# Optimization experiments

Hardware: AMD Instinct MI355X
Metric: run time of the kernel (lower is better)

## Reference

```python
import jax, jax.numpy as jnp
import numpy as np
from jax import lax

B = 8; IMG = 224; P = 16; D = 192; DEPTH = 8
H = IMG // P; W = H; L = H * W
D_IN = 384; D_STATE = 16; D_CONV = 4; DT_R = 12; NCLS = 1000
EPS = 1e-5


def _ln(x, w, b):
    m = x.mean(-1, keepdims=True)
    v = ((x - m) ** 2).mean(-1, keepdims=True)
    return (x - m) * lax.rsqrt(v + EPS) * w + b


def _mixer(seq, p):
    # seq: (B, L, D) -> Mamba selective-scan mixer
    xz = jnp.einsum('bld,ed->ble', seq, p['in_proj_w'])  # (B,L,2*D_IN)
    u, z = jnp.split(xz, 2, axis=-1)
    # causal depthwise conv1d over L
    uc = lax.conv_general_dilated(u.transpose(0, 2, 1), p['conv_w'][:, None, :], (1,),
                                  [(D_CONV - 1, 0)], feature_group_count=D_IN,
                                  dimension_numbers=('NCH', 'OIH', 'NCH'))
    u = jax.nn.silu(uc.transpose(0, 2, 1) + p['conv_b'])
    xdbl = jnp.einsum('bld,ed->ble', u, p['x_proj_w'])  # (B,L,DT_R+2*D_STATE)
    dt = xdbl[..., :DT_R]
    Bm = xdbl[..., DT_R:DT_R + D_STATE]
    Cm = xdbl[..., DT_R + D_STATE:]
    delta = jax.nn.softplus(jnp.einsum('blr,dr->bld', dt, p['dt_w']) + p['dt_b'])
    A = -jnp.exp(p['A_log'])  # (D_IN, D_STATE)

    def step(h, inp):
        d_t, B_t, C_t, u_t = inp  # (b,D_IN),(b,N),(b,N),(b,D_IN)
        h = h * jnp.exp(d_t[..., None] * A) + (d_t * u_t)[..., None] * B_t[:, None, :]
        return h, jnp.einsum('bdn,bn->bd', h, C_t)

    h0 = jnp.zeros((seq.shape[0], D_IN, D_STATE), seq.dtype)
    _, ys = lax.scan(step, h0, (delta.transpose(1, 0, 2), Bm.transpose(1, 0, 2),
                                Cm.transpose(1, 0, 2), u.transpose(1, 0, 2)))
    y = ys.transpose(1, 0, 2) + u * p['D']
    y = y * jax.nn.silu(z)
    return jnp.einsum('bld,cd->blc', y, p['out_proj_w'])


def _stack(seq, params):
    # Block: residual = residual + hidden; hidden = mixer(LN(residual))
    def body(carry, p):
        hidden, residual = carry
        residual = residual + hidden
        hidden = _mixer(_ln(residual, p['ln_w'], p['ln_b']), p)
        return (hidden, residual), None

    (hidden, residual), _ = lax.scan(body, (seq, jnp.zeros_like(seq)), params)
    return hidden + residual


def _forward(x, patch_w, patch_b, pe_ln_w, pe_ln_b, ln_w, ln_b, in_proj_w, conv_w,
             conv_b, x_proj_w, dt_w, dt_b, A_log, Dp, out_proj_w, out_norm_w,
             out_norm_b, head_ln_w, head_ln_b, head_w, head_b):
    b = x.shape[0]
    # patch embed: conv(stride=patch) + LayerNorm over channels
    feat = lax.conv_general_dilated(x, patch_w, (P, P), 'VALID',
                                    dimension_numbers=('NCHW', 'OIHW', 'NCHW'))
    feat = feat + patch_b[None, :, None, None]  # (B, D, H, W)
    feat = _ln(feat.transpose(0, 2, 3, 1), pe_ln_w, pe_ln_b).transpose(0, 3, 1, 2)
    # CrossScan: 4 directional unrollings
    x0 = feat.reshape(b, D, L)
    x1 = feat.transpose(0, 1, 3, 2).reshape(b, D, L)
    xs = jnp.stack([x0, x1, x0[..., ::-1], x1[..., ::-1]], axis=1)  # (B,4,D,L)
    dirs = xs.transpose(1, 0, 3, 2)  # (4,B,L,D)
    params = {'ln_w': ln_w, 'ln_b': ln_b, 'in_proj_w': in_proj_w, 'conv_w': conv_w,
              'conv_b': conv_b, 'x_proj_w': x_proj_w, 'dt_w': dt_w, 'dt_b': dt_b,
              'A_log': A_log, 'D': Dp, 'out_proj_w': out_proj_w}
    outs = jax.vmap(_stack)(dirs, params)  # (4,B,L,D)
    # CrossMerge
    ys = outs.transpose(1, 0, 3, 2)  # (B,4,D,L)
    ym = ys[:, 0:2] + ys[:, 2:4][..., ::-1]
    y = ym[:, 0] + ym[:, 1].reshape(b, D, W, H).transpose(0, 1, 3, 2).reshape(b, D, L)
    y = _ln(y.transpose(0, 2, 1), out_norm_w, out_norm_b)  # (B,L,D)
    y = _ln(y.reshape(b, H, W, D), head_ln_w, head_ln_b)
    return y.mean(axis=(1, 2)) @ head_w.T + head_b  # (B, NCLS)


def setup_inputs() -> dict:
    key = jax.random.key(0)
    ks = jax.random.split(key, 10)
    rn = lambda k, s, sc=0.02: jax.random.normal(k, s, jnp.float32) * sc
    A_init = jnp.broadcast_to(jnp.arange(1, D_STATE + 1, dtype=jnp.float32),
                              (4, DEPTH, D_IN, D_STATE))
    return {
        'x': jax.random.normal(ks[0], (B, 3, IMG, IMG), jnp.float32),
        'patch_w': rn(ks[1], (D, 3, P, P)),
        'patch_b': jnp.zeros((D,), jnp.float32),
        'pe_ln_w': jnp.ones((D,), jnp.float32),
        'pe_ln_b': jnp.zeros((D,), jnp.float32),
        'ln_w': jnp.ones((4, DEPTH, D), jnp.float32),
        'ln_b': jnp.zeros((4, DEPTH, D), jnp.float32),
        'in_proj_w': rn(ks[2], (4, DEPTH, 2 * D_IN, D)),
        'conv_w': rn(ks[3], (4, DEPTH, D_IN, D_CONV), 0.1),
        'conv_b': jnp.zeros((4, DEPTH, D_IN), jnp.float32),
        'x_proj_w': rn(ks[4], (4, DEPTH, DT_R + 2 * D_STATE, D_IN)),
        'dt_w': rn(ks[5], (4, DEPTH, D_IN, DT_R), 0.1),
        'dt_b': jnp.log(jnp.expm1(0.01)) + rn(ks[6], (4, DEPTH, D_IN), 0.02),
        'A_log': jnp.log(A_init),
        'Dp': jnp.ones((4, DEPTH, D_IN), jnp.float32),
        'out_proj_w': rn(ks[7], (4, DEPTH, D, D_IN)),
        'out_norm_w': jnp.ones((D,), jnp.float32),
        'out_norm_b': jnp.zeros((D,), jnp.float32),
        'head_ln_w': jnp.ones((D,), jnp.float32),
        'head_ln_b': jnp.zeros((D,), jnp.float32),
        'head_w': rn(ks[8], (NCLS, D)),
        'head_b': jnp.zeros((NCLS,), jnp.float32),
    }


def reference(x, patch_w, patch_b, pe_ln_w, pe_ln_b, ln_w, ln_b, in_proj_w, conv_w,
              conv_b, x_proj_w, dt_w, dt_b, A_log, Dp, out_proj_w, out_norm_w,
              out_norm_b, head_ln_w, head_ln_b, head_w, head_b):
    return _forward(x, patch_w, patch_b, pe_ln_w, pe_ln_b, ln_w, ln_b, in_proj_w,
                    conv_w, conv_b, x_proj_w, dt_w, dt_b, A_log, Dp, out_proj_w,
                    out_norm_w, out_norm_b, head_ln_w, head_ln_b, head_w, head_b)
```

## Files before the change

kernel.cpp:

```cpp
#include <hip/hip_runtime.h>

#define B_ 8
#define IMGSZ 224
#define PATCH 16
#define D_ 192
#define DEPTH_ 8
#define H_ 14
#define W_ 14
#define L_ 196
#define DIN 384
#define DSTATE 16
#define DCONV 4
#define DTR 12
#define NCLS_ 1000
#define EPS_ 1e-5f
#define ROWS_PER_DIR (B_*L_)
#define M_TOTAL (4*ROWS_PER_DIR)

typedef unsigned short ushort_t;
typedef unsigned int uint_t;
typedef __attribute__((ext_vector_type(8)))  short bf16x8;
typedef __attribute__((ext_vector_type(16))) float f32x16;

__device__ __forceinline__ ushort_t f2bf(float f) {
  uint_t u = __builtin_bit_cast(uint_t, f);
  u += 0x7fffu + ((u >> 16) & 1u);
  return (ushort_t)(u >> 16);
}
__device__ __forceinline__ float bf2f(ushort_t s) {
  uint_t u = ((uint_t)s) << 16;
  return __builtin_bit_cast(float, u);
}

__global__ __launch_bounds__(256) void k_cvt3(
    const float* __restrict__ s0, const float* __restrict__ s1,
    const float* __restrict__ s2, ushort_t* __restrict__ dst)
{
  int i = blockIdx.x*256 + threadIdx.x;
  if (i >= 1806336) return;
  const float* src;
  int off;
  if (i < 36864)        { src = s0; off = i; }
  else if (i < 1216512) { src = s1; off = i - 36864; }
  else                  { src = s2; off = i - 1216512; }
  float4 v = reinterpret_cast<const float4*>(src)[off];
  ushort4 o;
  o.x = f2bf(v.x); o.y = f2bf(v.y); o.z = f2bf(v.z); o.w = f2bf(v.w);
  reinterpret_cast<ushort4*>(dst)[i] = o;
}

__global__ __launch_bounds__(256) void k_cvt_xw(const float* __restrict__ src,
                                                ushort_t* __restrict__ dst)
{
  int idx = blockIdx.x*256 + threadIdx.x;
  if (idx >= 32*64*384) return;
  int g = idx / (64*384);
  int r = (idx / 384) % 64;
  int k = idx % 384;
  float v = (r < 44) ? src[((size_t)g*44 + r)*384 + k] : 0.f;
  dst[idx] = f2bf(v);
}

__global__ __launch_bounds__(256) void k_im2col(const float* __restrict__ x,
                                                ushort_t* __restrict__ Xp)
{
  int idx = blockIdx.x*256 + threadIdx.x;
  if (idx >= ROWS_PER_DIR*768) return;
  int row = idx / 768, k = idx - row*768;
  int b = row / L_, l = row - b*L_;
  int hh = l / W_, ww = l - hh*W_;
  int c = k >> 8, rem = k & 255, pi = rem >> 4, pj = rem & 15;
  float v = x[(((size_t)b*3 + c)*IMGSZ + hh*PATCH + pi)*IMGSZ + ww*PATCH + pj];
  Xp[idx] = f2bf(v);
}

template<int KT, int OBF>
__global__ __launch_bounds__(64) void k_gemm2(
    const ushort_t* __restrict__ X, const ushort_t* __restrict__ W,
    void* __restrict__ C, int N, int nb, int wstride, int rows_per_dir)
{
  int row0 = blockIdx.x*32, col0 = blockIdx.y*64;
  int dir = row0 / rows_per_dir;
  const ushort_t* Wp = W + (size_t)dir*wstride;
  int l = threadIdx.x;
  int r31 = l & 31, khalf = (l >> 5)*8;
  const ushort_t* aptr  = X  + (size_t)(row0 + r31)*KT + khalf;
  const ushort_t* b0ptr = Wp + (size_t)(col0 + r31)*KT + khalf;
  const ushort_t* b1ptr = b0ptr + (size_t)32*KT;
  f32x16 acc00 = {}, acc01 = {}, acc10 = {}, acc11 = {};
  #pragma unroll
  for (int k = 0; k < KT; k += 32) {
    bf16x8 a0 = *reinterpret_cast<const bf16x8*>(aptr + k);
    bf16x8 a1 = *reinterpret_cast<const bf16x8*>(aptr + k + 16);
    bf16x8 b00 = *reinterpret_cast<const bf16x8*>(b0ptr + k);
    bf16x8 b01 = *reinterpret_cast<const bf16x8*>(b0ptr + k + 16);
    bf16x8 b10 = *reinterpret_cast<const bf16x8*>(b1ptr + k);
    bf16x8 b11 = *reinterpret_cast<const bf16x8*>(b1ptr + k + 16);
    acc00 = __builtin_amdgcn_mfma_f32_32x32x16_bf16(a0, b00, acc00, 0, 0, 0);
    acc01 = __builtin_amdgcn_mfma_f32_32x32x16_bf16(a1, b01, acc01, 0, 0, 0);
    acc10 = __builtin_amdgcn_mfma_f32_32x32x16_bf16(a0, b10, acc10, 0, 0, 0);
    acc11 = __builtin_amdgcn_mfma_f32_32x32x16_bf16(a1, b11, acc11, 0, 0, 0);
  }
  int c0 = col0 + r31, c1 = col0 + 32 + r31;
  #pragma unroll
  for (int r = 0; r < 16; ++r) {
    int row = (r & 3) + 8*(r >> 2) + 4*(l >> 5);
    size_t base = (size_t)(row0 + row)*N;
    float v0 = acc00[r] + acc01[r];
    float v1 = acc10[r] + acc11[r];
    if (OBF) {
      ushort_t* crow = (ushort_t*)C + base;
      if (c0 < nb) crow[c0] = f2bf(v0);
      if (c1 < nb) crow[c1] = f2bf(v1);
    } else {
      float* crow = (float*)C + base;
      if (c0 < nb) crow[c0] = v0;
      if (c1 < nb) crow[c1] = v1;
    }
  }
}

__global__ __launch_bounds__(64) void k_peln(
    const float* __restrict__ Cp, const float* __restrict__ pb,
    const float* __restrict__ plw, const float* __restrict__ plb,
    const float* __restrict__ lnw, const float* __restrict__ lnb,
    float* __restrict__ residual, ushort_t* __restrict__ xln)
{
  int blk = blockIdx.x;
  int b = blk / L_, l = blk - b*L_;
  int hh = l / W_, ww = l - hh*W_;
  int lane = threadIdx.x;
  float v[3]; float s = 0.f;
  #pragma unroll
  for (int i = 0; i < 3; ++i) {
    int d = lane + i*64;
    float t = Cp[(size_t)blk*D_ + d] + pb[d];
    v[i] = t; s += t;
  }
  #pragma unroll
  for (int off = 32; off; off >>= 1) s += __shfl_xor(s, off);
  float m = s*(1.f/D_); float q = 0.f;
  #pragma unroll
  for (int i = 0; i < 3; ++i) { float dd = v[i]-m; q += dd*dd; }
  #pragma unroll
  for (int off = 32; off; off >>= 1) q += __shfl_xor(q, off);
  float inv = rsqrtf(q*(1.f/D_)+EPS_);
  float nv[3]; s = 0.f;
  #pragma unroll
  for (int i = 0; i < 3; ++i) {
    int d = lane + i*64;
    nv[i] = (v[i]-m)*inv*plw[d] + plb[d];
    s += nv[i];
  }
  #pragma unroll
  for (int off = 32; off; off >>= 1) s += __shfl_xor(s, off);
  float m2 = s*(1.f/D_); q = 0.f;
  #pragma unroll
  for (int i = 0; i < 3; ++i) { float dd = nv[i]-m2; q += dd*dd; }
  #pragma unroll
  for (int off = 32; off; off >>= 1) q += __shfl_xor(q, off);
  float inv2 = rsqrtf(q*(1.f/D_)+EPS_);
  int l1 = ww*W_ + hh;
  size_t rr[4];
  rr[0] = ((size_t)(0*B_+b))*L_ + l;
  rr[1] = ((size_t)(1*B_+b))*L_ + l1;
  rr[2] = ((size_t)(2*B_+b))*L_ + (L_-1-l);
  rr[3] = ((size_t)(3*B_+b))*L_ + (L_-1-l1);
  #pragma unroll
  for (int i = 0; i < 3; ++i) {
    int d = lane + i*64;
    float nrm = (nv[i]-m2)*inv2;
    #pragma unroll
    for (int k = 0; k < 4; ++k) {
      residual[rr[k]*D_+d] = nv[i];
      xln[rr[k]*D_+d] = f2bf(nrm*lnw[(size_t)(k*DEPTH_)*D_+d] + lnb[(size_t)(k*DEPTH_)*D_+d]);
    }
  }
}

__global__ __launch_bounds__(256) void k_conv(
    const ushort_t* __restrict__ xzb, const float* __restrict__ cw,
    const float* __restrict__ cb, ushort_t* __restrict__ ub, int layer)
{
  int idx = blockIdx.x*256 + threadIdx.x;
  if (idx >= M_TOTAL*48) return;
  int row = idx / 48, c8 = (idx - row*48)*8;
  int kdir = row / ROWS_PER_DIR;
  int l = row % L_;
  size_t pbase = (size_t)(kdir*DEPTH_+layer)*DIN + c8;
  float wv[32];
  #pragma unroll
  for (int i = 0; i < 8; ++i)
    ((float4*)wv)[i] = ((const float4*)(cw + pbase*DCONV))[i];
  float acc[8];
  #pragma unroll
  for (int i = 0; i < 2; ++i)
    ((float4*)acc)[i] = ((const float4*)(cb + pbase))[i];
  #pragma unroll
  for (int t = 0; t < DCONV; ++t) {
    int lt = l - 3 + t;
    if (lt >= 0) {
      bf16x8 xv = *reinterpret_cast<const bf16x8*>(xzb + (size_t)(row-3+t)*768 + c8);
      #pragma unroll
      for (int j = 0; j < 8; ++j)
        acc[j] += bf2f((ushort_t)xv[j]) * wv[j*4 + t];
    }
  }
  bf16x8 o;
  #pragma unroll
  for (int j = 0; j < 8; ++j) {
    float uv = acc[j] / (1.f + __expf(-acc[j]));
    o[j] = (short)f2bf(uv);
  }
  *reinterpret_cast<bf16x8*>(ub + (size_t)row*DIN + c8) = o;
}

#define SCHUNK 14
#define NCHUNK 14
__global__ __launch_bounds__(256, 3) void k_scan(
    const ushort_t* __restrict__ ub, const float* __restrict__ xdbl,
    const ushort_t* __restrict__ xzb,
    const float* __restrict__ Alog, const float* __restrict__ Dp,
    const float* __restrict__ dtw, const float* __restrict__ dtb,
    ushort_t* __restrict__ yg, int layer)
{
  int blk = blockIdx.x;
  int kdir = blk / (B_*24);
  int rem = blk % (B_*24);
  int b = rem / 24, dc = rem % 24;
  int tid = threadIdx.x;
  int st = tid & 15, ch = tid >> 4;
  size_t pl = (size_t)(kdir*DEPTH_+layer)*DIN + dc*16 + ch;
  float a = -expf(Alog[pl*DSTATE + st]);
  size_t rowbase = ((size_t)kdir*B_ + b)*L_;

  int ll = tid >> 4, cc = tid & 15;
  bool ldr = tid < 224;
  size_t plc = (size_t)(kdir*DEPTH_+layer)*DIN + dc*16 + cc;
  float Dv3 = Dp[plc];
  float dwt[12]; float dbias = dtb[plc];
  #pragma unroll
  for (int i = 0; i < 3; ++i)
    ((float4*)dwt)[i] = ((const float4*)(dtw + plc*DTR))[i];

  __shared__ __align__(16) float sd[16][20], su[16][20], sB[16][20],
                                 sC[16][20], sz[16][20];
  __shared__ __align__(16) float sp[SCHUNK][16][20];

  float rd=0.f, ru=0.f, rB=0.f, rC=0.f, rz=0.f;
  if (ldr) {
    size_t r = rowbase + ll;
    float xv[12];
    #pragma unroll
    for (int i = 0; i < 3; ++i) ((float4*)xv)[i] = ((const float4*)(xdbl + r*44))[i];
    float acc = dbias;
    #pragma unroll
    for (int t = 0; t < DTR; ++t) acc += xv[t]*dwt[t];
    rd = (acc > 20.f) ? acc : log1pf(__expf(acc));
    ru = bf2f(ub[r*DIN + dc*16 + cc]);
    rB = xdbl[r*44 + DTR + cc];
    rC = xdbl[r*44 + DTR + DSTATE + cc];
    rz = bf2f(xzb[r*768 + DIN + dc*16 + cc]);
  }

  float h = 0.f;
  for (int chk = 0; chk < NCHUNK; ++chk) {
    if (ldr) { sd[cc][ll]=rd; su[cc][ll]=ru; sB[cc][ll]=rB; sC[cc][ll]=rC; sz[cc][ll]=rz; }
    __syncthreads();
    if (chk+1 < NCHUNK && ldr) {
      size_t r = rowbase + (chk+1)*SCHUNK + ll;
      float xv[12];
      #pragma unroll
      for (int i = 0; i < 3; ++i) ((float4*)xv)[i] = ((const float4*)(xdbl + r*44))[i];
      float acc = dbias;
      #pragma unroll
      for (int t = 0; t < DTR; ++t) acc += xv[t]*dwt[t];
      rd = (acc > 20.f) ? acc : log1pf(__expf(acc));
      ru = bf2f(ub[r*DIN + dc*16 + cc]);
      rB = xdbl[r*44 + DTR + cc];
      rC = xdbl[r*44 + DTR + DSTATE + cc];
      rz = bf2f(xzb[r*768 + DIN + dc*16 + cc]);
    }
    float dlv[16], ulv[16], Bvv[16], Cvv[16];
    #pragma unroll
    for (int i = 0; i < 4; ++i) {
      ((float4*)dlv)[i] = ((const float4*)&sd[ch][0])[i];
      ((float4*)ulv)[i] = ((const float4*)&su[ch][0])[i];
      ((float4*)Bvv)[i] = ((const float4*)&sB[st][0])[i];
      ((float4*)Cvv)[i] = ((const float4*)&sC[st][0])[i];
    }
    float E[SCHUNK];
    #pragma unroll
    for (int l = 0; l < SCHUNK; ++l) E[l] = __expf(dlv[l]*a);
    #pragma unroll
    for (int l = 0; l < SCHUNK; ++l) {
      h = h*E[l] + dlv[l]*ulv[l]*Bvv[l];
      sp[l][ch][st] = h*Cvv[l];
    }
    __syncthreads();
    if (ldr) {
      float pv[16];
      #pragma unroll
      for (int i = 0; i < 4; ++i)
        ((float4*)pv)[i] = ((const float4*)&sp[ll][cc][0])[i];
      float s = 0.f;
      #pragma unroll
      for (int i = 0; i < 16; ++i) s += pv[i];
      float ul = su[cc][ll];
      float z  = sz[cc][ll];
      float yv = (s + ul*Dv3) * (z / (1.f + __expf(-z)));
      yg[(rowbase + chk*SCHUNK + ll)*DIN + dc*16 + cc] = f2bf(yv);
    }
    __syncthreads();
  }
}

template<int LAST>
__global__ __launch_bounds__(384) void k_outln(
    const ushort_t* __restrict__ X, const ushort_t* __restrict__ W,
    float* __restrict__ residual,
    const float* __restrict__ lnw, const float* __restrict__ lnb,
    ushort_t* __restrict__ xln, int layer)
{
  int row0 = blockIdx.x*32;
  int dir = row0 / ROWS_PER_DIR;
  const ushort_t* Wp = W + (size_t)dir*(DEPTH_*D_*DIN);
  int tid = threadIdx.x;
  int wv = tid >> 6;
  int l  = tid & 63;
  int col0 = wv*32;
  int r31 = l & 31, khalf = (l >> 5)*8;
  const ushort_t* aptr = X  + (size_t)(row0 + r31)*DIN + khalf;
  const ushort_t* bptr = Wp + (size_t)(col0 + r31)*DIN + khalf;
  f32x16 acc0 = {}, acc1 = {};
  #pragma unroll
  for (int k = 0; k < DIN; k += 32) {
    bf16x8 a0 = *reinterpret_cast<const bf16x8*>(aptr + k);
    bf16x8 b0 = *reinterpret_cast<const bf16x8*>(bptr + k);
    bf16x8 a1 = *reinterpret_cast<const bf16x8*>(aptr + k + 16);
    bf16x8 b1 = *reinterpret_cast<const bf16x8*>(bptr + k + 16);
    acc0 = __builtin_amdgcn_mfma_f32_32x32x16_bf16(a0, b0, acc0, 0, 0, 0);
    acc1 = __builtin_amdgcn_mfma_f32_32x32x16_bf16(a1, b1, acc1, 0, 0, 0);
  }
  __shared__ __align__(16) float Cs[32][196];
  __shared__ float sred[32][12], qred[32][12], sm[32], si[32];
  #pragma unroll
  for (int r = 0; r < 16; ++r) {
    int row = (r & 3) + 8*(r >> 2) + 4*(l >> 5);
    Cs[row][col0 + r31] = acc0[r] + acc1[r];
  }
  __syncthreads();
  int rr = tid / 12, jj = tid - rr*12;
  int c0 = jj*16;
  float* resrow = residual + (size_t)(row0+rr)*D_ + c0;
  float v[16];
  float s = 0.f, q = 0.f;
  #pragma unroll
  for (int i = 0; i < 16; i += 4) {
    float4 rv = *reinterpret_cast<const float4*>(resrow + i);
    float4 cv = *reinterpret_cast<const float4*>(&Cs[rr][c0 + i]);
    v[i+0] = rv.x + cv.x; v[i+1] = rv.y + cv.y;
    v[i+2] = rv.z + cv.z; v[i+3] = rv.w + cv.w;
  }
  #pragma unroll
  for (int i = 0; i < 16; ++i) { s += v[i]; q += v[i]*v[i]; }
  #pragma unroll
  for (int i = 0; i < 16; i += 4) {
    float4 o = make_float4(v[i], v[i+1], v[i+2], v[i+3]);
    *reinterpret_cast<float4*>(resrow + i) = o;
  }
  if (!LAST) {
    sred[rr][jj] = s; qred[rr][jj] = q;
    __syncthreads();
    if (tid < 32) {
      float S = 0.f, Q = 0.f;
      #pragma unroll
      for (int j = 0; j < 12; ++j) { S += sred[tid][j]; Q += qred[tid][j]; }
      float m = S*(1.f/D_);
      float var = Q*(1.f/D_) - m*m;
      sm[tid] = m; si[tid] = rsqrtf(var + EPS_);
    }
    __syncthreads();
    float m = sm[rr], inv = si[rr];
    const float* w = lnw + (size_t)(dir*DEPTH_ + layer + 1)*D_ + c0;
    const float* bb = lnb + (size_t)(dir*DEPTH_ + layer + 1)*D_ + c0;
    ushort_t* xrow = xln + (size_t)(row0+rr)*D_ + c0;
    #pragma unroll
    for (int i = 0; i < 16; ++i)
      xrow[i] = f2bf((v[i]-m)*inv*w[i] + bb[i]);
  }
}

__global__ __launch_bounds__(64) void k_combine(
    const float* __restrict__ res,
    const float* __restrict__ onw, const float* __restrict__ onb,
    const float* __restrict__ hlw, const float* __restrict__ hlb,
    float* __restrict__ ynorm)
{
  int blk = blockIdx.x;
  int b = blk / L_, l = blk % L_;
  int hh = l / W_, ww = l % W_;
  int l1 = ww*W_ + hh;
  size_t r0 = ((size_t)(0*B_+b))*L_ + l;
  size_t r1 = ((size_t)(1*B_+b))*L_ + l1;
  size_t r2 = ((size_t)(2*B_+b))*L_ + (L_-1-l);
  size_t r3 = ((size_t)(3*B_+b))*L_ + (L_-1-l1);
  int lane = threadIdx.x;
  float v[3]; float s = 0.f;
  #pragma unroll
  for (int i=0;i<3;i++){
    int d = lane + i*64;
    float t = res[r0*D_+d] + res[r1*D_+d] + res[r2*D_+d] + res[r3*D_+d];
    v[i]=t; s+=t;
  }
  #pragma unroll
  for (int off=32;off;off>>=1) s += __shfl_xor(s,off);
  float m = s*(1.f/D_); float q=0.f;
  #pragma unroll
  for (int i=0;i<3;i++){ float dd=v[i]-m; q+=dd*dd; }
  #pragma unroll
  for (int off=32;off;off>>=1) q += __shfl_xor(q,off);
  float inv = rsqrtf(q*(1.f/D_)+EPS_);
  float v2[3]; s = 0.f;
  #pragma unroll
  for (int i=0;i<3;i++){ int d=lane+i*64; float t=(v[i]-m)*inv*onw[d]+onb[d]; v2[i]=t; s+=t; }
  #pragma unroll
  for (int off=32;off;off>>=1) s += __shfl_xor(s,off);
  float m2 = s*(1.f/D_); q=0.f;
  #pragma unroll
  for (int i=0;i<3;i++){ float dd=v2[i]-m2; q+=dd*dd; }
  #pragma unroll
  for (int off=32;off;off>>=1) q += __shfl_xor(q,off);
  float inv2 = rsqrtf(q*(1.f/D_)+EPS_);
  #pragma unroll
  for (int i=0;i<3;i++){ int d=lane+i*64; ynorm[((size_t)b*L_+l)*D_+d] = (v2[i]-m2)*inv2*hlw[d]+hlb[d]; }
}

__global__ __launch_bounds__(192) void k_mean(const float* __restrict__ ynorm, float* __restrict__ ybar)
{
  int b = blockIdx.x, d = threadIdx.x;
  float s = 0.f;
  for (int l = 0; l < L_; ++l) s += ynorm[((size_t)b*L_+l)*D_ + d];
  ybar[b*D_+d] = s * (1.f/L_);
}

__global__ __launch_bounds__(256) void k_head(
    const float* __restrict__ ybar, const float* __restrict__ hw, const float* __restrict__ hb,
    float* __restrict__ out)
{
  __shared__ float ys[D_];
  int b = blockIdx.x >> 2;
  int c = (blockIdx.x & 3)*256 + threadIdx.x;
  for (int i = threadIdx.x; i < D_; i += 256) ys[i] = ybar[b*D_+i];
  __syncthreads();
  if (c < NCLS_) {
    float acc = hb[c];
    const float* wr = hw + (size_t)c*D_;
    for (int dd = 0; dd < D_; dd += 4) {
      float4 a4 = *reinterpret_cast<const float4*>(&ys[dd]);
      float4 b4 = *reinterpret_cast<const float4*>(&wr[dd]);
      acc += a4.x*b4.x + a4.y*b4.y + a4.z*b4.z + a4.w*b4.w;
    }
    out[(size_t)b*NCLS_ + c] = acc;
  }
}

extern "C" void kernel_launch(void* const* d_in, const int* in_sizes, int n_in,
                              void* d_out, int out_size, void* d_ws, size_t ws_size,
                              hipStream_t stream)
{
  const float* x          = (const float*)d_in[0];
  const float* patch_w    = (const float*)d_in[1];
  const float* patch_b    = (const float*)d_in[2];
  const float* pe_ln_w    = (const float*)d_in[3];
  const float* pe_ln_b    = (const float*)d_in[4];
  const float* ln_w       = (const float*)d_in[5];
  const float* ln_b       = (const float*)d_in[6];
  const float* in_proj_w  = (const float*)d_in[7];
  const float* conv_w     = (const float*)d_in[8];
  const float* conv_b     = (const float*)d_in[9];
  const float* x_proj_w   = (const float*)d_in[10];
  const float* dt_w       = (const float*)d_in[11];
  const float* dt_b       = (const float*)d_in[12];
  const float* A_log      = (const float*)d_in[13];
  const float* Dp         = (const float*)d_in[14];
  const float* out_proj_w = (const float*)d_in[15];
  const float* out_norm_w = (const float*)d_in[16];
  const float* out_norm_b = (const float*)d_in[17];
  const float* head_ln_w  = (const float*)d_in[18];
  const float* head_ln_b  = (const float*)d_in[19];
  const float* head_w     = (const float*)d_in[20];
  const float* head_b     = (const float*)d_in[21];
  float* out = (float*)d_out;

  float* ws = (float*)d_ws;
  float*    residual = ws;
  ushort_t* xz_bf    = (ushort_t*)(residual + 1204224);
  ushort_t* u_bf     = xz_bf + 4816896;
  float*    xdbl     = (float*)(u_bf + 2408448);
  ushort_t* yg_bf    = (ushort_t*)(xdbl + 275968);
  ushort_t* xln_bf   = yg_bf + 2408448;
  ushort_t* wbf      = xln_bf + 1204224;
  ushort_t* pw_bf    = wbf;
  ushort_t* inw_bf   = wbf + 147456;
  ushort_t* outw_bf  = inw_bf + 4718592;
  ushort_t* xw_bf    = outw_bf + 2359296;
  ushort_t* Xp       = xz_bf;
  float*    C_patch  = (float*)(xz_bf + 1204224);
  float*    ynorm    = (float*)yg_bf;
  float*    ybar     = ynorm + 301056;

  k_cvt3<<<(1806336+255)/256, 256, 0, stream>>>(patch_w, in_proj_w, out_proj_w, wbf);
  k_cvt_xw<<<(32*64*384+255)/256, 256, 0, stream>>>(x_proj_w, xw_bf);

  k_im2col<<<(ROWS_PER_DIR*768+255)/256, 256, 0, stream>>>(x, Xp);
  k_gemm2<768,0><<<dim3(ROWS_PER_DIR/32, 3), 64, 0, stream>>>(
      Xp, pw_bf, C_patch, D_, D_, 0, ROWS_PER_DIR);
  k_peln<<<ROWS_PER_DIR, 64, 0, stream>>>(C_patch, patch_b, pe_ln_w, pe_ln_b,
                                          ln_w, ln_b, residual, xln_bf);

  for (int layer = 0; layer < DEPTH_; ++layer) {
    k_gemm2<192,1><<<dim3(M_TOTAL/32, 12), 64, 0, stream>>>(
        xln_bf, inw_bf + (size_t)layer*768*D_, xz_bf, 768, 768, DEPTH_*768*D_, ROWS_PER_DIR);
    k_conv<<<(M_TOTAL*48+255)/256, 256, 0, stream>>>(xz_bf, conv_w, conv_b, u_bf, layer);
    k_gemm2<384,0><<<dim3(M_TOTAL/32, 1), 64, 0, stream>>>(
        u_bf, xw_bf + (size_t)layer*64*384, xdbl, 44, 44, DEPTH_*64*384, ROWS_PER_DIR);
    k_scan<<<4*B_*24, 256, 0, stream>>>(
        u_bf, xdbl, xz_bf, A_log, Dp, dt_w, dt_b, yg_bf, layer);
    if (layer < DEPTH_-1)
      k_outln<0><<<M_TOTAL/32, 384, 0, stream>>>(
          yg_bf, outw_bf, residual, ln_w, ln_b, xln_bf, layer);
    else
      k_outln<1><<<M_TOTAL/32, 384, 0, stream>>>(
          yg_bf, outw_bf, residual, ln_w, ln_b, xln_bf, layer);
  }

  k_combine<<<B_*L_, 64, 0, stream>>>(residual, out_norm_w, out_norm_b,
                                      head_ln_w, head_ln_b, ynorm);
  k_mean<<<B_, 192, 0, stream>>>(ynorm, ybar);
  k_head<<<B_*4, 256, 0, stream>>>(ybar, head_w, head_b, out);
}
```

Measured before the change: 703.1 us.

## Fuse causal conv with x_proj GEMM and double-buffer scan shared staging

Merges the depthwise conv+SiLU kernel with the x_proj MFMA GEMM into one kernel per 32-row tile, so u is consumed right after it is produced and one launch per layer goes away. The scan kernel's per-chunk shared staging arrays are double-buffered, which removes the trailing barrier in each chunk iteration. The risks are that only half the waves do the fused GEMM, and that u is re-read through global memory inside the block.

```diff
diff --git a/kernel.cpp b/kernel.cpp
--- a/kernel.cpp
+++ b/kernel.cpp
@@ -178,41 +178,75 @@
   }
 }
 
-__global__ __launch_bounds__(256) void k_conv(
+__global__ __launch_bounds__(256) void k_convxp(
     const ushort_t* __restrict__ xzb, const float* __restrict__ cw,
-    const float* __restrict__ cb, ushort_t* __restrict__ ub, int layer)
-{
-  int idx = blockIdx.x*256 + threadIdx.x;
-  if (idx >= M_TOTAL*48) return;
-  int row = idx / 48, c8 = (idx - row*48)*8;
-  int kdir = row / ROWS_PER_DIR;
-  int l = row % L_;
-  size_t pbase = (size_t)(kdir*DEPTH_+layer)*DIN + c8;
-  float wv[32];
-  #pragma unroll
-  for (int i = 0; i < 8; ++i)
-    ((float4*)wv)[i] = ((const float4*)(cw + pbase*DCONV))[i];
-  float acc[8];
-  #pragma unroll
-  for (int i = 0; i < 2; ++i)
-    ((float4*)acc)[i] = ((const float4*)(cb + pbase))[i];
-  #pragma unroll
-  for (int t = 0; t < DCONV; ++t) {
-    int lt = l - 3 + t;
-    if (lt >= 0) {
-      bf16x8 xv = *reinterpret_cast<const bf16x8*>(xzb + (size_t)(row-3+t)*768 + c8);
+    const float* __restrict__ cb, const ushort_t* __restrict__ xw,
+    ushort_t* __restrict__ ub, float* __restrict__ xdbl, int layer)
+{
+  int row0 = blockIdx.x*32;
+  int dir = row0 / ROWS_PER_DIR;
+  int tid = threadIdx.x;
+  #pragma unroll
+  for (int it = 0; it < 6; ++it) {
+    int wi = it*256 + tid;
+    int r = wi / 48, g = wi - r*48;
+    int c8 = g*8;
+    int row = row0 + r;
+    int l = row % L_;
+    size_t pbase = (size_t)(dir*DEPTH_+layer)*DIN + c8;
+    float wv[32];
+    #pragma unroll
+    for (int i = 0; i < 8; ++i)
+      ((float4*)wv)[i] = ((const float4*)(cw + pbase*DCONV))[i];
+    float acc[8];
+    #pragma unroll
+    for (int i = 0; i < 2; ++i)
+      ((float4*)acc)[i] = ((const float4*)(cb + pbase))[i];
+    #pragma unroll
+    for (int t = 0; t < DCONV; ++t) {
+      int lt = l - 3 + t;
+      if (lt >= 0) {
+        bf16x8 xv = *reinterpret_cast<const bf16x8*>(xzb + (size_t)(row-3+t)*768 + c8);
+        #pragma unroll
+        for (int j = 0; j < 8; ++j)
+          acc[j] += bf2f((ushort_t)xv[j]) * wv[j*4 + t];
+      }
+    }
+    bf16x8 o;
+    #pragma unroll
+    for (int j = 0; j < 8; ++j) {
+      float uv = acc[j] / (1.f + __expf(-acc[j]));
+      o[j] = (short)f2bf(uv);
+    }
+    *reinterpret_cast<bf16x8*>(ub + (size_t)row*DIN + c8) = o;
+  }
+  __syncthreads();
+  int wv_ = tid >> 6;
+  if (wv_ < 2) {
+    int l = tid & 63;
+    int r31 = l & 31, khalf = (l >> 5)*8;
+    const ushort_t* aptr = ub + (size_t)(row0 + r31)*DIN + khalf;
+    const ushort_t* bptr = xw + (size_t)(dir*DEPTH_+layer)*64*384
+                              + (size_t)(wv_*32 + r31)*384 + khalf;
+    f32x16 acc0 = {}, acc1 = {};
+    #pragma unroll
+    for (int k = 0; k < DIN; k += 32) {
+      bf16x8 a0 = *reinterpret_cast<const bf16x8*>(aptr + k);
+      bf16x8 b0 = *reinterpret_cast<const bf16x8*>(bptr + k);
+      bf16x8 a1 = *reinterpret_cast<const bf16x8*>(aptr + k + 16);
+      bf16x8 b1 = *reinterpret_cast<const bf16x8*>(bptr + k + 16);
+      acc0 = __builtin_amdgcn_mfma_f32_32x32x16_bf16(a0, b0, acc0, 0, 0, 0);
+      acc1 = __builtin_amdgcn_mfma_f32_32x32x16_bf16(a1, b1, acc1, 0, 0, 0);
+    }
+    int c = wv_*32 + r31;
+    if (c < 44) {
       #pragma unroll
-      for (int j = 0; j < 8; ++j)
-        acc[j] += bf2f((ushort_t)xv[j]) * wv[j*4 + t];
-    }
-  }
-  bf16x8 o;
-  #pragma unroll
-  for (int j = 0; j < 8; ++j) {
-    float uv = acc[j] / (1.f + __expf(-acc[j]));
-    o[j] = (short)f2bf(uv);
-  }
-  *reinterpret_cast<bf16x8*>(ub + (size_t)row*DIN + c8) = o;
+      for (int r = 0; r < 16; ++r) {
+        int rr = (r & 3) + 8*(r >> 2) + 4*(l >> 5);
+        xdbl[(size_t)(row0 + rr)*44 + c] = acc0[r] + acc1[r];
+      }
+    }
+  }
 }
 
 #define SCHUNK 14
@@ -243,8 +277,8 @@
   for (int i = 0; i < 3; ++i)
     ((float4*)dwt)[i] = ((const float4*)(dtw + plc*DTR))[i];
 
-  __shared__ __align__(16) float sd[16][20], su[16][20], sB[16][20],
-                                 sC[16][20], sz[16][20];
+  __shared__ __align__(16) float sd[2][16][20], su[2][16][20], sB[2][16][20],
+                                 sC[2][16][20], sz[2][16][20];
   __shared__ __align__(16) float sp[SCHUNK][16][20];
 
   float rd=0.f, ru=0.f, rB=0.f, rC=0.f, rz=0.f;
@@ -264,8 +298,10 @@
   }
 
   float h = 0.f;
+  int cur = 0;
   for (int chk = 0; chk < NCHUNK; ++chk) {
-    if (ldr) { sd[cc][ll]=rd; su[cc][ll]=ru; sB[cc][ll]=rB; sC[cc][ll]=rC; sz[cc][ll]=rz; }
+    if (ldr) { sd[cur][cc][ll]=rd; su[cur][cc][ll]=ru; sB[cur][cc][ll]=rB;
+               sC[cur][cc][ll]=rC; sz[cur][cc][ll]=rz; }
     __syncthreads();
     if (chk+1 < NCHUNK && ldr) {
       size_t r = rowbase + (chk+1)*SCHUNK + ll;
@@ -284,10 +320,10 @@
     float dlv[16], ulv[16], Bvv[16], Cvv[16];
     #pragma unroll
     for (int i = 0; i < 4; ++i) {
-      ((float4*)dlv)[i] = ((const float4*)&sd[ch][0])[i];
-      ((float4*)ulv)[i] = ((const float4*)&su[ch][0])[i];
-      ((float4*)Bvv)[i] = ((const float4*)&sB[st][0])[i];
-      ((float4*)Cvv)[i] = ((const float4*)&sC[st][0])[i];
+      ((float4*)dlv)[i] = ((const float4*)&sd[cur][ch][0])[i];
+      ((float4*)ulv)[i] = ((const float4*)&su[cur][ch][0])[i];
+      ((float4*)Bvv)[i] = ((const float4*)&sB[cur][st][0])[i];
+      ((float4*)Cvv)[i] = ((const float4*)&sC[cur][st][0])[i];
     }
     float E[SCHUNK];
     #pragma unroll
@@ -306,12 +342,12 @@
       float s = 0.f;
       #pragma unroll
       for (int i = 0; i < 16; ++i) s += pv[i];
-      float ul = su[cc][ll];
-      float z  = sz[cc][ll];
+      float ul = su[cur][cc][ll];
+      float z  = sz[cur][cc][ll];
       float yv = (s + ul*Dv3) * (z / (1.f + __expf(-z)));
       yg[(rowbase + chk*SCHUNK + ll)*DIN + dc*16 + cc] = f2bf(yv);
     }
-    __syncthreads();
+    cur ^= 1;
   }
 }
 
@@ -522,9 +558,8 @@
   for (int layer = 0; layer < DEPTH_; ++layer) {
     k_gemm2<192,1><<<dim3(M_TOTAL/32, 12), 64, 0, stream>>>(
         xln_bf, inw_bf + (size_t)layer*768*D_, xz_bf, 768, 768, DEPTH_*768*D_, ROWS_PER_DIR);
-    k_conv<<<(M_TOTAL*48+255)/256, 256, 0, stream>>>(xz_bf, conv_w, conv_b, u_bf, layer);
-    k_gemm2<384,0><<<dim3(M_TOTAL/32, 1), 64, 0, stream>>>(
-        u_bf, xw_bf + (size_t)layer*64*384, xdbl, 44, 44, DEPTH_*64*384, ROWS_PER_DIR);
+    k_convxp<<<M_TOTAL/32, 256, 0, stream>>>(
+        xz_bf, conv_w, conv_b, xw_bf, u_bf, xdbl, layer);
     k_scan<<<4*B_*24, 256, 0, stream>>>(
         u_bf, xdbl, xz_bf, A_log, Dp, dt_w, dt_b, yg_bf, layer);
     if (layer < DEPTH_-1)
```

Result: slower. 720.5 us (+2.5%).
